# Kernel optimization log

Hardware: AMD Instinct MI355X
Metric: run time of the kernel (lower is better)

Reference implementation:

```python
import jax, jax.numpy as jnp
import numpy as np

D_MODEL = 1024
N_HEADS = 16
D_HEAD = D_MODEL // N_HEADS
B, S = 2, 2048


def setup_inputs() -> dict:
    key = jax.random.key(0)
    ks = jax.random.split(key, 8)
    scale = 1.0 / np.sqrt(D_MODEL)
    return {
        "x": jax.random.normal(ks[0], (B, S, D_MODEL), dtype=jnp.float32),
        "Wq": jax.random.normal(ks[1], (D_MODEL, D_MODEL), dtype=jnp.float32) * scale,
        "bq": jnp.zeros((D_MODEL,), dtype=jnp.float32),
        "Wk": jax.random.normal(ks[2], (D_MODEL, D_MODEL), dtype=jnp.float32) * scale,
        "bk": jnp.zeros((D_MODEL,), dtype=jnp.float32),
        "Wv": jax.random.normal(ks[3], (D_MODEL, D_MODEL), dtype=jnp.float32) * scale,
        "bv": jnp.zeros((D_MODEL,), dtype=jnp.float32),
        "Wo": jax.random.normal(ks[4], (D_MODEL, D_MODEL), dtype=jnp.float32) * scale,
    }


def reference(x, Wq, bq, Wk, bk, Wv, bv, Wo):
    Bsz, Slen, D = x.shape
    # projections -> [B, H, S, Dh]
    def split_heads(t):
        return t.reshape(Bsz, Slen, N_HEADS, D_HEAD).transpose(0, 2, 1, 3)
    q = split_heads(x @ Wq + bq)
    k = split_heads(x @ Wk + bk)
    v = split_heads(x @ Wv + bv)
    scale = jnp.sqrt(jnp.float32(D_HEAD))
    scores = jnp.einsum('bhsd,bhtd->bhst', q, k) / scale  # [B,H,S,S]
    causal_mask = jnp.tril(jnp.ones((Slen, Slen), dtype=jnp.bool_))
    scores = jnp.where(causal_mask, scores, jnp.finfo(scores.dtype).min)
    attn = jax.nn.softmax(scores, axis=-1)
    # deterministic=True path: dropout is identity
    out = jnp.einsum('bhst,bhtd->bhsd', attn, v)
    out = out.transpose(0, 2, 1, 3).reshape(Bsz, Slen, D)
    return out @ Wo
```

## Files before the change

kernel.cpp:

```cpp
#include <hip/hip_runtime.h>
#include <hip/hip_bf16.h>

#define BATCH   2
#define SEQ     2048
#define DMODEL  1024
#define NHEADS  16
#define DHEAD   64
#define MROWS   (BATCH*SEQ)

typedef float  f32x4  __attribute__((ext_vector_type(4)));
typedef short  s16x4  __attribute__((ext_vector_type(4)));
typedef __bf16 bf16x8 __attribute__((ext_vector_type(8)));

__device__ __forceinline__ short f2bf(float f) {
  union { float f; unsigned u; } v; v.f = f;
  return (short)((v.u + 0x7fffu + ((v.u >> 16) & 1u)) >> 16);
}

__global__ void convert_x(const float* __restrict__ x, short* __restrict__ xb) {
  int i = (blockIdx.x * 256 + threadIdx.x) * 4;
  float4 v = *(const float4*)(x + i);
  s16x4 o = { f2bf(v.x), f2bf(v.y), f2bf(v.z), f2bf(v.w) };
  *(s16x4*)(xb + i) = o;
}

__global__ void transpose_w(const float* __restrict__ Wq, const float* __restrict__ Wk,
                            const float* __restrict__ Wv, const float* __restrict__ Wo,
                            short* __restrict__ WtQKV, short* __restrict__ WtO) {
  __shared__ float t[32][33];
  const float* W; short* Wt;
  int z = blockIdx.z;
  if      (z == 0) { W = Wq; Wt = WtQKV; }
  else if (z == 1) { W = Wk; Wt = WtQKV + (1u << 20); }
  else if (z == 2) { W = Wv; Wt = WtQKV + (2u << 20); }
  else             { W = Wo; Wt = WtO; }
  int n0 = blockIdx.x * 32, k0 = blockIdx.y * 32;
  int tx = threadIdx.x, ty = threadIdx.y;
  #pragma unroll
  for (int i = 0; i < 32; i += 8) t[ty + i][tx] = W[(k0 + ty + i) * DMODEL + n0 + tx];
  __syncthreads();
  #pragma unroll
  for (int i = 0; i < 32; i += 8) Wt[(n0 + ty + i) * DMODEL + k0 + tx] = f2bf(t[tx][ty + i]);
}

__global__ void transpose_v(const short* __restrict__ vb, short* __restrict__ vt) {
  __shared__ short t[64][65];
  int bh = blockIdx.x, s0 = blockIdx.y * 64;
  const short* src = vb + (bh * SEQ + s0) * DHEAD;
  short* dst = vt + bh * DHEAD * SEQ;
  int tid = threadIdx.x;
  #pragma unroll
  for (int i = 0; i < 16; i++) {
    int idx = tid + i * 256;
    t[idx >> 6][idx & 63] = src[idx];
  }
  __syncthreads();
  #pragma unroll
  for (int i = 0; i < 16; i++) {
    int idx = tid + i * 256;
    int d = idx >> 6, s = idx & 63;
    dst[d * SEQ + s0 + s] = t[s][d];
  }
}

template<int MT, int NT, int EPI>
__global__ __launch_bounds__(256) void gemm_bf16(
    const short* __restrict__ A, const short* __restrict__ Bt,
    const float* __restrict__ bq, const float* __restrict__ bk, const float* __restrict__ bv,
    short* __restrict__ qb, short* __restrict__ kb, short* __restrict__ vb,
    float* __restrict__ out)
{
  constexpr int K = DMODEL, BK = 32;
  constexpr int WM = MT / 2, WN = NT / 2;
  constexpr int TM = WM / 16, TN = WN / 16;
  constexpr int CA = MT * BK / 512;
  constexpr int CB = NT * BK / 512;
  __shared__ short la[MT * BK];
  __shared__ short lb[NT * BK];
  const int tid = threadIdx.x;
  const int wave = tid >> 6, lane = tid & 63;
  const int quad = lane >> 4, l16 = lane & 15;
  const int wr = wave >> 1, wc = wave & 1;
  const int m0 = blockIdx.y * MT, n0 = blockIdx.x * NT;
  const int arow = lane >> 2, acol = (lane & 3) * 8;

  f32x4 acc[TM][TN] = {};

  for (int k0 = 0; k0 < K; k0 += BK) {
    for (int c = wave; c < CA; c += 4) {
      const short* gp = A + (m0 + c * 16 + arow) * K + k0 + acol;
      __builtin_amdgcn_global_load_lds((__attribute__((address_space(1))) void*)gp,
                                       (__attribute__((address_space(3))) void*)(la + c * 512),
                                       16, 0, 0);
    }
    for (int c = wave; c < CB; c += 4) {
      const short* gp = Bt + (n0 + c * 16 + arow) * K + k0 + acol;
      __builtin_amdgcn_global_load_lds((__attribute__((address_space(1))) void*)gp,
                                       (__attribute__((address_space(3))) void*)(lb + c * 512),
                                       16, 0, 0);
    }
    __syncthreads();
    bf16x8 af[TM], bfr[TN];
    #pragma unroll
    for (int i = 0; i < TM; ++i)
      af[i] = *(const bf16x8*)&la[(wr * WM + i * 16 + l16) * BK + quad * 8];
    #pragma unroll
    for (int j = 0; j < TN; ++j)
      bfr[j] = *(const bf16x8*)&lb[(wc * WN + j * 16 + l16) * BK + quad * 8];
    #pragma unroll
    for (int i = 0; i < TM; ++i)
      #pragma unroll
      for (int j = 0; j < TN; ++j)
        acc[i][j] = __builtin_amdgcn_mfma_f32_16x16x32_bf16(af[i], bfr[j], acc[i][j], 0, 0, 0);
    __syncthreads();
  }

  if constexpr (EPI == 0) {
    const float* bias; short* dst; int nbase; float scl;
    if (n0 < DMODEL)          { bias = bq; dst = qb; nbase = 0;          scl = 0.125f * 1.44269504089f; }
    else if (n0 < 2 * DMODEL) { bias = bk; dst = kb; nbase = DMODEL;     scl = 1.f; }
    else                      { bias = bv; dst = vb; nbase = 2 * DMODEL; scl = 1.f; }
    #pragma unroll
    for (int j = 0; j < TN; ++j) {
      int col = n0 - nbase + wc * WN + j * 16 + l16;
      float bias_v = bias[col];
      int hd = (col >> 6) * (SEQ * DHEAD) + (col & 63);
      #pragma unroll
      for (int i = 0; i < TM; ++i)
        #pragma unroll
        for (int r = 0; r < 4; ++r) {
          int mrow = m0 + wr * WM + i * 16 + quad * 4 + r;
          int b = mrow >> 11, s = mrow & (SEQ - 1);
          dst[b * (NHEADS * SEQ * DHEAD) + hd + s * DHEAD] = f2bf((acc[i][j][r] + bias_v) * scl);
        }
    }
  } else {
    #pragma unroll
    for (int i = 0; i < TM; ++i)
      #pragma unroll
      for (int r = 0; r < 4; ++r) {
        int mrow = m0 + wr * WM + i * 16 + quad * 4 + r;
        #pragma unroll
        for (int j = 0; j < TN; ++j)
          out[mrow * DMODEL + n0 + wc * WN + j * 16 + l16] = acc[i][j][r];
      }
    (void)bq; (void)bk; (void)bv; (void)qb; (void)kb; (void)vb;
  }
}


__global__ __launch_bounds__(256, 2) void attn_k(
    const short* __restrict__ qbp, const short* __restrict__ kbp,
    const short* __restrict__ vtb, short* __restrict__ ob)
{
  __shared__ short kls[2][4096];
  __shared__ short vls[2][4096];
  const int tid = threadIdx.x, wave = tid >> 6, lane = tid & 63;
  const int quad = lane >> 4, l16 = lane & 15;
  const int bh = blockIdx.x >> 4;
  const int qg = blockIdx.x & 15;
  const int qt = qg * 4 + wave;
  const int ma = qt * 16;
  const int mb = (127 - qt) * 16;
  const int nch = ((127 - qg * 4) * 16) / 64 + 1;
  const short* Q  = qbp + bh * SEQ * DHEAD;
  const short* Kp = kbp + bh * SEQ * DHEAD;
  const short* Vt = vtb + bh * DHEAD * SEQ;

  bf16x8 qa0 = *(const bf16x8*)&Q[(ma + l16) * DHEAD + quad * 8];
  bf16x8 qa1 = *(const bf16x8*)&Q[(ma + l16) * DHEAD + 32 + quad * 8];
  bf16x8 qb0 = *(const bf16x8*)&Q[(mb + l16) * DHEAD + quad * 8];
  bf16x8 qb1 = *(const bf16x8*)&Q[(mb + l16) * DHEAD + 32 + quad * 8];

  float lA = 0.f, lB = 0.f;
  f32x4 oA[4] = {}, oB[4] = {};

  const int vdl = lane >> 3, vsl = lane & 7;

  auto stage = [&](int buf, int t0) {
    #pragma unroll
    for (int j = 0; j < 2; ++j) {
      int g = j * 4 + wave;
      const short* gp = Kp + (t0 + lane) * DHEAD + g * 8;
      __builtin_amdgcn_global_load_lds((__attribute__((address_space(1))) void*)gp,
                                       (__attribute__((address_space(3))) void*)&kls[buf][g * 512],
                                       16, 0, 0);
    }
    #pragma unroll
    for (int j = 0; j < 2; ++j) {
      int gd = j * 4 + wave;
      const short* gp = Vt + (gd * 8 + vdl) * SEQ + t0 + ((vsl ^ vdl) * 8);
      __builtin_amdgcn_global_load_lds((__attribute__((address_space(1))) void*)gp,
                                       (__attribute__((address_space(3))) void*)&vls[buf][gd * 512],
                                       16, 0, 0);
    }
  };

  auto frag = [&](const bf16x8 kf[4][2], const s16x4 vf[4][4], int t0, int mF,
                  bf16x8 f0, bf16x8 f1, float& lF, f32x4 oF[4]) {
    const int nlive = (mF - t0) / 16 + 1;
    #pragma unroll
    for (int t = 0; t < 4; ++t) {
      if (t < nlive) {
        f32x4 a = {};
        a = __builtin_amdgcn_mfma_f32_16x16x32_bf16(kf[t][0], f0, a, 0, 0, 0);
        a = __builtin_amdgcn_mfma_f32_16x16x32_bf16(kf[t][1], f1, a, 0, 0, 0);
        if (t0 + t * 16 == mF) {
          #pragma unroll
          for (int r = 0; r < 4; ++r)
            if (quad * 4 + r > l16) a[r] = -1e30f;
        }
        f32x4 p;
        #pragma unroll
        for (int r = 0; r < 4; ++r) p[r] = __builtin_amdgcn_exp2f(a[r]);
        lF += (p[0] + p[1]) + (p[2] + p[3]);
        __hip_bfloat162 c01 = __float22bfloat162_rn(float2{p[0], p[1]});
        __hip_bfloat162 c23 = __float22bfloat162_rn(float2{p[2], p[3]});
        union { unsigned u[2]; s16x4 s; } pu;
        pu.u[0] = *(unsigned*)&c01; pu.u[1] = *(unsigned*)&c23;
        #pragma unroll
        for (int dt = 0; dt < 4; ++dt)
          oF[dt] = __builtin_amdgcn_mfma_f32_16x16x16bf16_1k(pu.s, vf[t][dt], oF[dt], 0, 0, 0);
      }
    }
  };

  stage(0, 0);
  for (int c = 0; c < nch; ++c) {
    __syncthreads();
    if (c + 1 < nch) stage((c + 1) & 1, (c + 1) * 64);
    const int t0 = c * 64;
    const int buf = c & 1;
    bf16x8 kf[4][2];
    #pragma unroll
    for (int t = 0; t < 4; ++t)
      #pragma unroll
      for (int h = 0; h < 2; ++h)
        kf[t][h] = *(const bf16x8*)&kls[buf][((h * 4 + quad) * 64 + t * 16 + l16) * 8];
    s16x4 vf[4][4];
    #pragma unroll
    for (int t = 0; t < 4; ++t) {
      int gsw = ((t * 2 + (quad >> 1)) ^ (l16 & 7));
      #pragma unroll
      for (int dt = 0; dt < 4; ++dt)
        vf[t][dt] = *(const s16x4*)&vls[buf][((dt * 16 + l16) * 8 + gsw) * 8 + (quad & 1) * 4];
    }
    if (t0 <= mb) frag(kf, vf, t0, mb, qb0, qb1, lB, oB);
    if (t0 <= ma) frag(kf, vf, t0, ma, qa0, qa1, lA, oA);
  }

  lA += __shfl_xor(lA, 16, 64); lA += __shfl_xor(lA, 32, 64);
  lB += __shfl_xor(lB, 16, 64); lB += __shfl_xor(lB, 32, 64);
  const int b = bh >> 4, h = bh & 15;
  #pragma unroll
  for (int r = 0; r < 4; ++r) {
    float liA = 1.0f / __shfl(lA, quad * 4 + r, 64);
    float liB = 1.0f / __shfl(lB, quad * 4 + r, 64);
    int sA = ma + quad * 4 + r, sB = mb + quad * 4 + r;
    #pragma unroll
    for (int dt = 0; dt < 4; ++dt) {
      ob[(b * SEQ + sA) * DMODEL + h * DHEAD + dt * 16 + l16] = f2bf(oA[dt][r] * liA);
      ob[(b * SEQ + sB) * DMODEL + h * DHEAD + dt * 16 + l16] = f2bf(oB[dt][r] * liB);
    }
  }
}

extern "C" void kernel_launch(void* const* d_in, const int* in_sizes, int n_in,
                              void* d_out, int out_size, void* d_ws, size_t ws_size,
                              hipStream_t stream) {
  const float* x  = (const float*)d_in[0];
  const float* Wq = (const float*)d_in[1];
  const float* bq = (const float*)d_in[2];
  const float* Wk = (const float*)d_in[3];
  const float* bk = (const float*)d_in[4];
  const float* Wv = (const float*)d_in[5];
  const float* bv = (const float*)d_in[6];
  const float* Wo = (const float*)d_in[7];
  float* out = (float*)d_out;

  char* ws = (char*)d_ws;
  short* xb  = (short*)(ws);
  short* wtq = (short*)(ws + (8u  << 20));
  short* wto = (short*)(ws + (14u << 20));
  short* qb  = (short*)(ws + (16u << 20));
  short* kb  = (short*)(ws + (24u << 20));
  short* vb  = (short*)(ws + (32u << 20));
  short* vt  = (short*)(ws + (40u << 20));
  short* ob  = (short*)(ws + (48u << 20));

  convert_x<<<MROWS * DMODEL / 1024, 256, 0, stream>>>(x, xb);
  transpose_w<<<dim3(32, 32, 4), dim3(32, 8), 0, stream>>>(Wq, Wk, Wv, Wo, wtq, wto);

  gemm_bf16<128, 128, 0><<<dim3(3 * DMODEL / 128, MROWS / 128), 256, 0, stream>>>(
      xb, wtq, bq, bk, bv, qb, kb, vb, nullptr);

  transpose_v<<<dim3(BATCH * NHEADS, SEQ / 64), 256, 0, stream>>>(vb, vt);

  attn_k<<<BATCH * NHEADS * 16, 256, 0, stream>>>(qb, kb, vt, ob);

  gemm_bf16<64, 128, 1><<<dim3(DMODEL / 128, MROWS / 64), 256, 0, stream>>>(
      ob, wto, nullptr, nullptr, nullptr, nullptr, nullptr, nullptr, out);
}
```

Baseline: 202.0 us.

## Fuse V transpose into QKV GEMM epilogue and shrink attention blocks

```diff
diff --git a/kernel.cpp b/kernel.cpp
--- a/kernel.cpp
+++ b/kernel.cpp
@@ -10,6 +10,7 @@
 
 typedef float  f32x4  __attribute__((ext_vector_type(4)));
 typedef short  s16x4  __attribute__((ext_vector_type(4)));
+typedef short  s16x8  __attribute__((ext_vector_type(8)));
 typedef __bf16 bf16x8 __attribute__((ext_vector_type(8)));
 
 __device__ __forceinline__ short f2bf(float f) {
@@ -43,31 +44,11 @@
   for (int i = 0; i < 32; i += 8) Wt[(n0 + ty + i) * DMODEL + k0 + tx] = f2bf(t[tx][ty + i]);
 }
 
-__global__ void transpose_v(const short* __restrict__ vb, short* __restrict__ vt) {
-  __shared__ short t[64][65];
-  int bh = blockIdx.x, s0 = blockIdx.y * 64;
-  const short* src = vb + (bh * SEQ + s0) * DHEAD;
-  short* dst = vt + bh * DHEAD * SEQ;
-  int tid = threadIdx.x;
-  #pragma unroll
-  for (int i = 0; i < 16; i++) {
-    int idx = tid + i * 256;
-    t[idx >> 6][idx & 63] = src[idx];
-  }
-  __syncthreads();
-  #pragma unroll
-  for (int i = 0; i < 16; i++) {
-    int idx = tid + i * 256;
-    int d = idx >> 6, s = idx & 63;
-    dst[d * SEQ + s0 + s] = t[s][d];
-  }
-}
-
 template<int MT, int NT, int EPI>
 __global__ __launch_bounds__(256) void gemm_bf16(
     const short* __restrict__ A, const short* __restrict__ Bt,
     const float* __restrict__ bq, const float* __restrict__ bk, const float* __restrict__ bv,
-    short* __restrict__ qb, short* __restrict__ kb, short* __restrict__ vb,
+    short* __restrict__ qb, short* __restrict__ kb, short* __restrict__ vt,
     float* __restrict__ out)
 {
   constexpr int K = DMODEL, BK = 32;
@@ -75,8 +56,11 @@
   constexpr int TM = WM / 16, TN = WN / 16;
   constexpr int CA = MT * BK / 512;
   constexpr int CB = NT * BK / 512;
-  __shared__ short la[MT * BK];
-  __shared__ short lb[NT * BK];
+  constexpr int TP = 136;
+  constexpr int SME = (EPI == 0) ? 128 * TP : (MT * BK + NT * BK);
+  __shared__ short smem[SME];
+  short* la = smem;
+  short* lb = smem + MT * BK;
   const int tid = threadIdx.x;
   const int wave = tid >> 6, lane = tid & 63;
   const int quad = lane >> 4, l16 = lane & 15;
@@ -116,23 +100,48 @@
   }
 
   if constexpr (EPI == 0) {
-    const float* bias; short* dst; int nbase; float scl;
-    if (n0 < DMODEL)          { bias = bq; dst = qb; nbase = 0;          scl = 0.125f * 1.44269504089f; }
-    else if (n0 < 2 * DMODEL) { bias = bk; dst = kb; nbase = DMODEL;     scl = 1.f; }
-    else                      { bias = bv; dst = vb; nbase = 2 * DMODEL; scl = 1.f; }
+    const bool isV = (n0 >= 2 * DMODEL);
+    const float* bias; int nbase; float scl;
+    if (n0 < DMODEL)          { bias = bq; nbase = 0;          scl = 0.125f * 1.44269504089f; }
+    else if (n0 < 2 * DMODEL) { bias = bk; nbase = DMODEL;     scl = 1.f; }
+    else                      { bias = bv; nbase = 2 * DMODEL; scl = 1.f; }
     #pragma unroll
     for (int j = 0; j < TN; ++j) {
-      int col = n0 - nbase + wc * WN + j * 16 + l16;
-      float bias_v = bias[col];
-      int hd = (col >> 6) * (SEQ * DHEAD) + (col & 63);
-      #pragma unroll
-      for (int i = 0; i < TM; ++i)
+      int coll = wc * WN + j * 16 + l16;
+      float bias_v = bias[n0 - nbase + coll];
+      #pragma unroll
+      for (int i = 0; i < TM; ++i) {
+        int rowl = wr * WM + i * 16 + quad * 4;
         #pragma unroll
         for (int r = 0; r < 4; ++r) {
-          int mrow = m0 + wr * WM + i * 16 + quad * 4 + r;
-          int b = mrow >> 11, s = mrow & (SEQ - 1);
-          dst[b * (NHEADS * SEQ * DHEAD) + hd + s * DHEAD] = f2bf((acc[i][j][r] + bias_v) * scl);
+          short v = f2bf((acc[i][j][r] + bias_v) * scl);
+          if (isV) smem[coll * TP + rowl + r] = v;
+          else     smem[(rowl + r) * TP + coll] = v;
         }
+      }
+    }
+    __syncthreads();
+    const int b = m0 >> 11, s0 = m0 & (SEQ - 1);
+    const int rseg = tid & 15, rrow = tid >> 4;
+    if (!isV) {
+      short* dst = (n0 < DMODEL) ? qb : kb;
+      #pragma unroll
+      for (int it = 0; it < 8; ++it) {
+        int row = it * 16 + rrow;
+        int colg = (n0 - nbase) + rseg * 8;
+        int h = colg >> 6, d = colg & 63;
+        s16x8 v = *(const s16x8*)&smem[row * TP + rseg * 8];
+        *(s16x8*)(dst + ((b * NHEADS + h) * SEQ + s0 + row) * DHEAD + d) = v;
+      }
+    } else {
+      #pragma unroll
+      for (int it = 0; it < 8; ++it) {
+        int drow = it * 16 + rrow;
+        int colg = (n0 - nbase) + drow;
+        int h = colg >> 6, d = colg & 63;
+        s16x8 v = *(const s16x8*)&smem[drow * TP + rseg * 8];
+        *(s16x8*)(vt + ((b * NHEADS + h) * DHEAD + d) * SEQ + s0 + rseg * 8) = v;
+      }
     }
   } else {
     #pragma unroll
@@ -144,12 +153,12 @@
         for (int j = 0; j < TN; ++j)
           out[mrow * DMODEL + n0 + wc * WN + j * 16 + l16] = acc[i][j][r];
       }
-    (void)bq; (void)bk; (void)bv; (void)qb; (void)kb; (void)vb;
+    (void)bq; (void)bk; (void)bv; (void)qb; (void)kb; (void)vt;
   }
 }
 
 
-__global__ __launch_bounds__(256, 2) void attn_k(
+__global__ __launch_bounds__(128, 2) void attn_k(
     const short* __restrict__ qbp, const short* __restrict__ kbp,
     const short* __restrict__ vtb, short* __restrict__ ob)
 {
@@ -157,12 +166,12 @@
   __shared__ short vls[2][4096];
   const int tid = threadIdx.x, wave = tid >> 6, lane = tid & 63;
   const int quad = lane >> 4, l16 = lane & 15;
-  const int bh = blockIdx.x >> 4;
-  const int qg = blockIdx.x & 15;
-  const int qt = qg * 4 + wave;
+  const int bh = blockIdx.x >> 5;
+  const int qg = blockIdx.x & 31;
+  const int qt = qg * 2 + wave;
   const int ma = qt * 16;
   const int mb = (127 - qt) * 16;
-  const int nch = ((127 - qg * 4) * 16) / 64 + 1;
+  const int nch = (127 - qg * 2) / 4 + 1;
   const short* Q  = qbp + bh * SEQ * DHEAD;
   const short* Kp = kbp + bh * SEQ * DHEAD;
   const short* Vt = vtb + bh * DHEAD * SEQ;
@@ -179,16 +188,16 @@
 
   auto stage = [&](int buf, int t0) {
     #pragma unroll
-    for (int j = 0; j < 2; ++j) {
-      int g = j * 4 + wave;
+    for (int j = 0; j < 4; ++j) {
+      int g = j * 2 + wave;
       const short* gp = Kp + (t0 + lane) * DHEAD + g * 8;
       __builtin_amdgcn_global_load_lds((__attribute__((address_space(1))) void*)gp,
                                        (__attribute__((address_space(3))) void*)&kls[buf][g * 512],
                                        16, 0, 0);
     }
     #pragma unroll
-    for (int j = 0; j < 2; ++j) {
-      int gd = j * 4 + wave;
+    for (int j = 0; j < 4; ++j) {
+      int gd = j * 2 + wave;
       const short* gp = Vt + (gd * 8 + vdl) * SEQ + t0 + ((vsl ^ vdl) * 8);
       __builtin_amdgcn_global_load_lds((__attribute__((address_space(1))) void*)gp,
                                        (__attribute__((address_space(3))) void*)&vls[buf][gd * 512],
@@ -284,19 +293,16 @@
   short* wto = (short*)(ws + (14u << 20));
   short* qb  = (short*)(ws + (16u << 20));
   short* kb  = (short*)(ws + (24u << 20));
-  short* vb  = (short*)(ws + (32u << 20));
-  short* vt  = (short*)(ws + (40u << 20));
-  short* ob  = (short*)(ws + (48u << 20));
+  short* vt  = (short*)(ws + (32u << 20));
+  short* ob  = (short*)(ws + (40u << 20));
 
   convert_x<<<MROWS * DMODEL / 1024, 256, 0, stream>>>(x, xb);
   transpose_w<<<dim3(32, 32, 4), dim3(32, 8), 0, stream>>>(Wq, Wk, Wv, Wo, wtq, wto);
 
   gemm_bf16<128, 128, 0><<<dim3(3 * DMODEL / 128, MROWS / 128), 256, 0, stream>>>(
-      xb, wtq, bq, bk, bv, qb, kb, vb, nullptr);
-
-  transpose_v<<<dim3(BATCH * NHEADS, SEQ / 64), 256, 0, stream>>>(vb, vt);
-
-  attn_k<<<BATCH * NHEADS * 16, 256, 0, stream>>>(qb, kb, vt, ob);
+      xb, wtq, bq, bk, bv, qb, kb, vt, nullptr);
+
+  attn_k<<<BATCH * NHEADS * 32, 128, 0, stream>>>(qb, kb, vt, ob);
 
   gemm_bf16<64, 128, 1><<<dim3(DMODEL / 128, MROWS / 64), 256, 0, stream>>>(
       ob, wto, nullptr, nullptr, nullptr, nullptr, nullptr, nullptr, out);
```

New measurement: 207.0 us. 2.5% more time.
